# Kernel optimization log

Measured on AMD Instinct MI355X. Metric: run time of the kernel, lower is better.

## Reference

```python
import jax, jax.numpy as jnp
import numpy as np
from jax.scipy.special import logsumexp

TEMPERATURE = 0.1
NEG_INF = -1e30


def _l2_normalize(x, eps=1e-12):
    # matches torch F.normalize(dim=1)
    n = jnp.sqrt(jnp.sum(x * x, axis=1, keepdims=True))
    return x / jnp.maximum(n, eps)


def _half_loss(out0, out1, diag):
    # sim matrices [N, N]
    sim_00 = jnp.einsum('nc,mc->nm', out0, out0) / TEMPERATURE
    sim_01 = jnp.einsum('nc,mc->nm', out0, out1) / TEMPERATURE
    positive_loss = -jnp.diagonal(sim_01)            # [N]
    # off-diagonal logsumexp per row (mask diag with -inf)
    neg_00 = logsumexp(jnp.where(diag, NEG_INF, sim_00), axis=1)
    neg_01 = logsumexp(jnp.where(diag, NEG_INF, sim_01), axis=1)
    return positive_loss.mean() + (neg_01 + neg_00).mean()


def setup_inputs() -> dict:
    key = jax.random.key(0)
    k0, k1 = jax.random.split(key)
    N, C = 8192, 128
    return {
        'img_rep': jax.random.normal(k0, (N, C), dtype=jnp.float32),
        'mol_rep': jax.random.normal(k1, (N, C), dtype=jnp.float32),
    }


def reference(img_rep, mol_rep):
    img = _l2_normalize(img_rep)
    mol = _l2_normalize(mol_rep)
    n = img.shape[0]
    diag = jnp.eye(n, dtype=bool)
    loss0 = _half_loss(img, mol, diag)  # mol_from_img
    loss1 = _half_loss(mol, img, diag)  # img_from_mol
    return 0.5 * (loss0 + loss1)
```

## Files before the change

### kernel.cpp

```cpp
#include <hip/hip_runtime.h>
#include <hip/hip_bf16.h>

typedef __attribute__((ext_vector_type(8))) short short8;
typedef __attribute__((ext_vector_type(4))) float floatx4;

#define N_ROWS 8192
#define C_DIM  128
#define CHUNK  512
#define NIT    (CHUNK / 64)
#define KSCALE 14.426950408889634f
#define LN2    0.6931471805599453f

__device__ __forceinline__ unsigned int pack_bf16x2(float x, float y) {
    union { float f; unsigned int u; } a, b;
    a.f = x; b.f = y;
    unsigned int ra = a.u + 0x7FFFu + ((a.u >> 16) & 1u);
    unsigned int rb = b.u + 0x7FFFu + ((b.u >> 16) & 1u);
    return (ra >> 16) | ((rb >> 16) << 16);
}
__device__ __forceinline__ float bf2f(unsigned short s) {
    union { unsigned int u; float f; } x; x.u = ((unsigned int)s) << 16;
    return x.f;
}

__global__ __launch_bounds__(256) void norm_kernel(
    const float* __restrict__ img, const float* __restrict__ mol,
    unsigned short* __restrict__ W, float* __restrict__ SE,
    float* __restrict__ out)
{
    if (blockIdx.x < 32) {
        int t = blockIdx.x * 1024 + threadIdx.x;
        SE[t] = 0.f; SE[t + 256] = 0.f; SE[t + 512] = 0.f; SE[t + 768] = 0.f;
        if (blockIdx.x == 0 && threadIdx.x == 0) *out = 0.f;
    }
    int wave = threadIdx.x >> 6, lane = threadIdx.x & 63;
    int row = blockIdx.x * 4 + wave;
    const float* src = (row < N_ROWS) ? (img + (size_t)row * C_DIM)
                                      : (mol + (size_t)(row - N_ROWS) * C_DIM);
    float2 v = *reinterpret_cast<const float2*>(src + lane * 2);
    float ss = v.x * v.x + v.y * v.y;
    #pragma unroll
    for (int m = 1; m < 64; m <<= 1) ss += __shfl_xor(ss, m);
    float inv = rsqrtf(ss);
    ((unsigned int*)(W + (size_t)row * C_DIM))[lane] =
        pack_bf16x2(v.x * inv, v.y * inv);
}

__global__ __launch_bounds__(256) void pass_kernel(
    const unsigned short* __restrict__ W, float* __restrict__ SE)
{
    __shared__ unsigned short buf[2][64][128];
    __shared__ float colbuf[CHUNK];

    int idx = blockIdx.x;
    const unsigned short *X, *Y;
    float *rowSE, *colSE;
    bool dual;
    int rb, ch;
    if (idx < 1024) {
        rb = idx >> 4; ch = idx & 15;
        X = W; Y = W + (size_t)N_ROWS * C_DIM;
        rowSE = SE + 1 * N_ROWS; colSE = SE + 3 * N_ROWS; dual = true;
    } else {
        int j = idx - 1024;
        const unsigned short* M = (j < 544) ? W : W + (size_t)N_ROWS * C_DIM;
        float* S = (j < 544) ? SE : SE + 2 * N_ROWS;
        if (j >= 544) j -= 544;
        X = M; Y = M; rowSE = S; colSE = S;
        if (j < 64) { rb = j; ch = rb >> 2; dual = false; }
        else {
            int j2 = j - 64, p = j2 >> 2;
            int si = 0, cum = 15;
            while (p >= cum) { p -= cum; ++si; cum = 15 - si; }
            int sj = si + 1 + p;
            rb = si * 4 + (j2 & 3); ch = sj; dual = true;
        }
    }

    int lane = threadIdx.x & 63, wave = threadIdx.x >> 6;
    int l15 = lane & 15, lg = lane >> 4;
    int rbase = rb * 128 + wave * 32;
    int cstart = ch * CHUNK;

    short8 af[2][4];
    #pragma unroll
    for (int m = 0; m < 2; ++m)
        #pragma unroll
        for (int k = 0; k < 4; ++k)
            af[m][k] = *reinterpret_cast<const short8*>(
                X + (size_t)(rbase + m * 16 + l15) * C_DIM + k * 32 + lg * 8);

    auto stage = [&](int bsel, int jb) {
        #pragma unroll
        for (int i = 0; i < 4; ++i) {
            int c = i * 4 + wave;
            int r = c * 4 + lg;
            int s = l15 ^ (r & 7);
            const void* gsrc = (const char*)Y + (size_t)(cstart + jb + r) * 256 + s * 16;
            void* ldst = (char*)&buf[bsel][0][0] + c * 1024;
            __builtin_amdgcn_global_load_lds(
                (const __attribute__((address_space(1))) unsigned int*)gsrc,
                (__attribute__((address_space(3))) unsigned int*)ldst,
                16, 0, 0);
        }
    };

    for (int c = threadIdx.x; c < CHUNK; c += 256) colbuf[c] = 0.f;

    float se[2][4] = {{0.f,0.f,0.f,0.f},{0.f,0.f,0.f,0.f}};

    stage(0, 0);
    int cur = 0;
    for (int it = 0; it < NIT; ++it) {
        if (it + 1 < NIT) {
            stage(cur ^ 1, (it + 1) * 64);
            asm volatile("s_waitcnt vmcnt(4)" ::: "memory");
        } else {
            asm volatile("s_waitcnt vmcnt(0)" ::: "memory");
        }
        __builtin_amdgcn_s_barrier();
        asm volatile("" ::: "memory");

        float ce[4] = {0.f, 0.f, 0.f, 0.f};
        #pragma unroll
        for (int n = 0; n < 4; ++n) {
            short8 bk[4];
            #pragma unroll
            for (int k = 0; k < 4; ++k) {
                int row = n * 16 + l15;
                int s = (k * 4 + lg) ^ (l15 & 7);
                bk[k] = *reinterpret_cast<const short8*>(
                    (const char*)&buf[cur][0][0] + row * 256 + s * 16);
            }
            #pragma unroll
            for (int m = 0; m < 2; ++m) {
                floatx4 acc = {0.f, 0.f, 0.f, 0.f};
                #pragma unroll
                for (int k = 0; k < 4; ++k)
                    acc = __builtin_amdgcn_mfma_f32_16x16x32_bf16(
                              af[m][k], bk[k], acc, 0, 0, 0);
                #pragma unroll
                for (int r = 0; r < 4; ++r) {
                    float e = __builtin_amdgcn_exp2f(acc[r] * KSCALE - KSCALE);
                    se[m][r] += e;
                    ce[n] += e;
                }
            }
        }
        if (dual) {
            #pragma unroll
            for (int n = 0; n < 4; ++n) {
                float c2 = ce[n];
                c2 += __shfl_xor(c2, 16);
                c2 += __shfl_xor(c2, 32);
                if (lg == 0)
                    atomicAdd(&colbuf[it * 64 + n * 16 + l15], c2);
            }
        }
        asm volatile("s_waitcnt lgkmcnt(0)" ::: "memory");
        __builtin_amdgcn_sched_barrier(0);
        __builtin_amdgcn_s_barrier();
        cur ^= 1;
    }

    #pragma unroll
    for (int m = 0; m < 2; ++m)
        #pragma unroll
        for (int r = 0; r < 4; ++r) {
            float s = se[m][r];
            s += __shfl_xor(s, 1);
            s += __shfl_xor(s, 2);
            s += __shfl_xor(s, 4);
            s += __shfl_xor(s, 8);
            if (l15 == 0)
                atomicAdd(&rowSE[rbase + m * 16 + lg * 4 + r], s);
        }
    __syncthreads();
    if (dual)
        for (int c = threadIdx.x; c < CHUNK; c += 256)
            atomicAdd(&colSE[cstart + c], colbuf[c]);
}

__global__ __launch_bounds__(256) void finalize_kernel(
    const unsigned short* __restrict__ W, const float* __restrict__ SE,
    float* __restrict__ out)
{
    __shared__ float partial[4];
    int lane = threadIdx.x & 63, wave = threadIdx.x >> 6;
    int row = blockIdx.x * 4 + wave;
    const unsigned short* a = W + (size_t)row * C_DIM;
    const unsigned short* b = W + (size_t)(N_ROWS + row) * C_DIM;
    float a0 = bf2f(a[lane * 2]), a1 = bf2f(a[lane * 2 + 1]);
    float b0 = bf2f(b[lane * 2]), b1 = bf2f(b[lane * 2 + 1]);
    float d00 = a0 * a0 + a1 * a1;
    float d01 = a0 * b0 + a1 * b1;
    float d11 = b0 * b0 + b1 * b1;
    #pragma unroll
    for (int m = 1; m < 64; m <<= 1) {
        d00 += __shfl_xor(d00, m);
        d01 += __shfl_xor(d01, m);
        d11 += __shfl_xor(d11, m);
    }
    if (lane == 0) {
        float s0 = SE[0 * N_ROWS + row] - __builtin_amdgcn_exp2f(KSCALE * (d00 - 1.f));
        float s1 = SE[1 * N_ROWS + row] - __builtin_amdgcn_exp2f(KSCALE * (d01 - 1.f));
        float s2 = SE[2 * N_ROWS + row] - __builtin_amdgcn_exp2f(KSCALE * (d11 - 1.f));
        float s3 = SE[3 * N_ROWS + row] - __builtin_amdgcn_exp2f(KSCALE * (d01 - 1.f));
        float l0 = LN2 * __builtin_amdgcn_logf(s0) + 10.f;
        float l1 = LN2 * __builtin_amdgcn_logf(s1) + 10.f;
        float l2 = LN2 * __builtin_amdgcn_logf(s2) + 10.f;
        float l3 = LN2 * __builtin_amdgcn_logf(s3) + 10.f;
        partial[wave] = -10.f * d01 + 0.5f * (l0 + l1 + l2 + l3);
    }
    __syncthreads();
    if (threadIdx.x == 0)
        atomicAdd(out, (partial[0] + partial[1] + partial[2] + partial[3])
                         * (1.0f / N_ROWS));
}

extern "C" void kernel_launch(void* const* d_in, const int* in_sizes, int n_in,
                              void* d_out, int out_size, void* d_ws, size_t ws_size,
                              hipStream_t stream)
{
    const float* img = (const float*)d_in[0];
    const float* mol = (const float*)d_in[1];
    float* out = (float*)d_out;
    unsigned short* W = (unsigned short*)d_ws;
    float* SE = (float*)((char*)d_ws + (size_t)2 * N_ROWS * C_DIM * 2);

    norm_kernel<<<dim3(N_ROWS * 2 / 4), 256, 0, stream>>>(img, mol, W, SE, out);
    pass_kernel<<<dim3(1024 + 544 + 544), 256, 0, stream>>>(W, SE);
    finalize_kernel<<<dim3(N_ROWS / 4), 256, 0, stream>>>(W, SE, out);
}
```

Before: 153.4 us.

## Fuse finalize into pass kernel via last-block reduction and precompute diagonals

Removes the separate finalize kernel: norm_kernel now handles img and mol rows together and computes the diagonal dot products into a D buffer, and the last pass block (found with an atomic counter) does the logsumexp finalization. Column sums go into per-wave LDS slots instead of LDS atomics, which also drops the colbuf zeroing and one barrier. The LDS swizzle widens from 8 to 16 slots to cut bank conflicts. The cost is a serial tail where a single block reduces all 8192 rows, plus one extra atomic and threadfence per block.

```diff
diff --git a/kernel.cpp b/kernel.cpp
--- a/kernel.cpp
+++ b/kernel.cpp
@@ -8,6 +8,7 @@
 #define C_DIM  128
 #define CHUNK  512
 #define NIT    (CHUNK / 64)
+#define NBLK   (1024 + 544 + 544)
 #define KSCALE 14.426950408889634f
 #define LN2    0.6931471805599453f
 
@@ -26,31 +27,56 @@
 __global__ __launch_bounds__(256) void norm_kernel(
     const float* __restrict__ img, const float* __restrict__ mol,
     unsigned short* __restrict__ W, float* __restrict__ SE,
-    float* __restrict__ out)
+    float* __restrict__ D, unsigned int* __restrict__ cnt)
 {
     if (blockIdx.x < 32) {
         int t = blockIdx.x * 1024 + threadIdx.x;
         SE[t] = 0.f; SE[t + 256] = 0.f; SE[t + 512] = 0.f; SE[t + 768] = 0.f;
-        if (blockIdx.x == 0 && threadIdx.x == 0) *out = 0.f;
+        if (blockIdx.x == 0 && threadIdx.x == 0) *cnt = 0u;
     }
     int wave = threadIdx.x >> 6, lane = threadIdx.x & 63;
     int row = blockIdx.x * 4 + wave;
-    const float* src = (row < N_ROWS) ? (img + (size_t)row * C_DIM)
-                                      : (mol + (size_t)(row - N_ROWS) * C_DIM);
-    float2 v = *reinterpret_cast<const float2*>(src + lane * 2);
-    float ss = v.x * v.x + v.y * v.y;
-    #pragma unroll
-    for (int m = 1; m < 64; m <<= 1) ss += __shfl_xor(ss, m);
-    float inv = rsqrtf(ss);
-    ((unsigned int*)(W + (size_t)row * C_DIM))[lane] =
-        pack_bf16x2(v.x * inv, v.y * inv);
+    float2 va = *reinterpret_cast<const float2*>(img + (size_t)row * C_DIM + lane * 2);
+    float2 vb = *reinterpret_cast<const float2*>(mol + (size_t)row * C_DIM + lane * 2);
+    float sa = va.x * va.x + va.y * va.y;
+    float sb = vb.x * vb.x + vb.y * vb.y;
+    #pragma unroll
+    for (int m = 1; m < 64; m <<= 1) {
+        sa += __shfl_xor(sa, m);
+        sb += __shfl_xor(sb, m);
+    }
+    float ia = rsqrtf(sa), ib = rsqrtf(sb);
+    unsigned int pa = pack_bf16x2(va.x * ia, va.y * ia);
+    unsigned int pb = pack_bf16x2(vb.x * ib, vb.y * ib);
+    ((unsigned int*)(W + (size_t)row * C_DIM))[lane] = pa;
+    ((unsigned int*)(W + (size_t)(N_ROWS + row) * C_DIM))[lane] = pb;
+    float a0 = bf2f((unsigned short)pa), a1 = bf2f((unsigned short)(pa >> 16));
+    float b0 = bf2f((unsigned short)pb), b1 = bf2f((unsigned short)(pb >> 16));
+    float d00 = a0 * a0 + a1 * a1;
+    float d01 = a0 * b0 + a1 * b1;
+    float d11 = b0 * b0 + b1 * b1;
+    #pragma unroll
+    for (int m = 1; m < 64; m <<= 1) {
+        d00 += __shfl_xor(d00, m);
+        d01 += __shfl_xor(d01, m);
+        d11 += __shfl_xor(d11, m);
+    }
+    if (lane == 0) {
+        D[row] = d00;
+        D[N_ROWS + row] = d01;
+        D[2 * N_ROWS + row] = d11;
+    }
 }
 
 __global__ __launch_bounds__(256) void pass_kernel(
-    const unsigned short* __restrict__ W, float* __restrict__ SE)
+    const unsigned short* __restrict__ W, float* __restrict__ SE,
+    const float* __restrict__ D, unsigned int* __restrict__ cnt,
+    float* __restrict__ out)
 {
     __shared__ unsigned short buf[2][64][128];
-    __shared__ float colbuf[CHUNK];
+    __shared__ float colbuf[4][CHUNK];
+    __shared__ bool islast;
+    __shared__ float red[4];
 
     int idx = blockIdx.x;
     const unsigned short *X, *Y;
@@ -95,7 +121,7 @@
         for (int i = 0; i < 4; ++i) {
             int c = i * 4 + wave;
             int r = c * 4 + lg;
-            int s = l15 ^ (r & 7);
+            int s = l15 ^ (r & 15);
             const void* gsrc = (const char*)Y + (size_t)(cstart + jb + r) * 256 + s * 16;
             void* ldst = (char*)&buf[bsel][0][0] + c * 1024;
             __builtin_amdgcn_global_load_lds(
@@ -104,8 +130,6 @@
                 16, 0, 0);
         }
     };
-
-    for (int c = threadIdx.x; c < CHUNK; c += 256) colbuf[c] = 0.f;
 
     float se[2][4] = {{0.f,0.f,0.f,0.f},{0.f,0.f,0.f,0.f}};
 
@@ -128,7 +152,7 @@
             #pragma unroll
             for (int k = 0; k < 4; ++k) {
                 int row = n * 16 + l15;
-                int s = (k * 4 + lg) ^ (l15 & 7);
+                int s = (k * 4 + lg) ^ l15;
                 bk[k] = *reinterpret_cast<const short8*>(
                     (const char*)&buf[cur][0][0] + row * 256 + s * 16);
             }
@@ -154,7 +178,7 @@
                 c2 += __shfl_xor(c2, 16);
                 c2 += __shfl_xor(c2, 32);
                 if (lg == 0)
-                    atomicAdd(&colbuf[it * 64 + n * 16 + l15], c2);
+                    colbuf[wave][it * 64 + n * 16 + l15] = c2;
             }
         }
         asm volatile("s_waitcnt lgkmcnt(0)" ::: "memory");
@@ -175,47 +199,44 @@
             if (l15 == 0)
                 atomicAdd(&rowSE[rbase + m * 16 + lg * 4 + r], s);
         }
-    __syncthreads();
     if (dual)
         for (int c = threadIdx.x; c < CHUNK; c += 256)
-            atomicAdd(&colSE[cstart + c], colbuf[c]);
-}
-
-__global__ __launch_bounds__(256) void finalize_kernel(
-    const unsigned short* __restrict__ W, const float* __restrict__ SE,
-    float* __restrict__ out)
-{
-    __shared__ float partial[4];
-    int lane = threadIdx.x & 63, wave = threadIdx.x >> 6;
-    int row = blockIdx.x * 4 + wave;
-    const unsigned short* a = W + (size_t)row * C_DIM;
-    const unsigned short* b = W + (size_t)(N_ROWS + row) * C_DIM;
-    float a0 = bf2f(a[lane * 2]), a1 = bf2f(a[lane * 2 + 1]);
-    float b0 = bf2f(b[lane * 2]), b1 = bf2f(b[lane * 2 + 1]);
-    float d00 = a0 * a0 + a1 * a1;
-    float d01 = a0 * b0 + a1 * b1;
-    float d11 = b0 * b0 + b1 * b1;
-    #pragma unroll
-    for (int m = 1; m < 64; m <<= 1) {
-        d00 += __shfl_xor(d00, m);
-        d01 += __shfl_xor(d01, m);
-        d11 += __shfl_xor(d11, m);
-    }
-    if (lane == 0) {
-        float s0 = SE[0 * N_ROWS + row] - __builtin_amdgcn_exp2f(KSCALE * (d00 - 1.f));
-        float s1 = SE[1 * N_ROWS + row] - __builtin_amdgcn_exp2f(KSCALE * (d01 - 1.f));
-        float s2 = SE[2 * N_ROWS + row] - __builtin_amdgcn_exp2f(KSCALE * (d11 - 1.f));
-        float s3 = SE[3 * N_ROWS + row] - __builtin_amdgcn_exp2f(KSCALE * (d01 - 1.f));
-        float l0 = LN2 * __builtin_amdgcn_logf(s0) + 10.f;
-        float l1 = LN2 * __builtin_amdgcn_logf(s1) + 10.f;
-        float l2 = LN2 * __builtin_amdgcn_logf(s2) + 10.f;
-        float l3 = LN2 * __builtin_amdgcn_logf(s3) + 10.f;
-        partial[wave] = -10.f * d01 + 0.5f * (l0 + l1 + l2 + l3);
-    }
+            atomicAdd(&colSE[cstart + c],
+                      colbuf[0][c] + colbuf[1][c] + colbuf[2][c] + colbuf[3][c]);
+
+    __syncthreads();
+    if (threadIdx.x == 0) {
+        __threadfence();
+        unsigned int old = atomicAdd(cnt, 1u);
+        islast = (old == NBLK - 1);
+    }
+    __syncthreads();
+    if (!islast) return;
+
+    float local = 0.f;
+    for (int r = threadIdx.x; r < N_ROWS; r += 256) {
+        float d00 = D[r], d01 = D[N_ROWS + r], d11 = D[2 * N_ROWS + r];
+        float e00 = __builtin_amdgcn_exp2f(KSCALE * (d00 - 1.f));
+        float e01 = __builtin_amdgcn_exp2f(KSCALE * (d01 - 1.f));
+        float e11 = __builtin_amdgcn_exp2f(KSCALE * (d11 - 1.f));
+        float s0 = __hip_atomic_load(&SE[r], __ATOMIC_RELAXED,
+                                     __HIP_MEMORY_SCOPE_AGENT) - e00;
+        float s1 = __hip_atomic_load(&SE[N_ROWS + r], __ATOMIC_RELAXED,
+                                     __HIP_MEMORY_SCOPE_AGENT) - e01;
+        float s2 = __hip_atomic_load(&SE[2 * N_ROWS + r], __ATOMIC_RELAXED,
+                                     __HIP_MEMORY_SCOPE_AGENT) - e11;
+        float s3 = __hip_atomic_load(&SE[3 * N_ROWS + r], __ATOMIC_RELAXED,
+                                     __HIP_MEMORY_SCOPE_AGENT) - e01;
+        float lg4 = __builtin_amdgcn_logf(s0) + __builtin_amdgcn_logf(s1)
+                  + __builtin_amdgcn_logf(s2) + __builtin_amdgcn_logf(s3);
+        local += -10.f * d01 + 0.5f * LN2 * lg4 + 20.f;
+    }
+    #pragma unroll
+    for (int m = 1; m < 64; m <<= 1) local += __shfl_xor(local, m);
+    if (lane == 0) red[wave] = local;
     __syncthreads();
     if (threadIdx.x == 0)
-        atomicAdd(out, (partial[0] + partial[1] + partial[2] + partial[3])
-                         * (1.0f / N_ROWS));
+        *out = (red[0] + red[1] + red[2] + red[3]) * (1.0f / N_ROWS);
 }
 
 extern "C" void kernel_launch(void* const* d_in, const int* in_sizes, int n_in,
@@ -226,9 +247,11 @@
     const float* mol = (const float*)d_in[1];
     float* out = (float*)d_out;
     unsigned short* W = (unsigned short*)d_ws;
-    float* SE = (float*)((char*)d_ws + (size_t)2 * N_ROWS * C_DIM * 2);
-
-    norm_kernel<<<dim3(N_ROWS * 2 / 4), 256, 0, stream>>>(img, mol, W, SE, out);
-    pass_kernel<<<dim3(1024 + 544 + 544), 256, 0, stream>>>(W, SE);
-    finalize_kernel<<<dim3(N_ROWS / 4), 256, 0, stream>>>(W, SE, out);
-}
+    char* base = (char*)d_ws + (size_t)2 * N_ROWS * C_DIM * 2;
+    float* SE = (float*)base;
+    float* D  = (float*)(base + 4 * N_ROWS * sizeof(float));
+    unsigned int* cnt = (unsigned int*)(base + 7 * N_ROWS * sizeof(float));
+
+    norm_kernel<<<dim3(N_ROWS / 4), 256, 0, stream>>>(img, mol, W, SE, D, cnt);
+    pass_kernel<<<dim3(NBLK), 256, 0, stream>>>(W, SE, D, cnt, out);
+}
```

Result: slower. 159.9 us (+4.2%).
